# Optimization experiments

Hardware: AMD Instinct MI355X
Metric: run time of the kernel (lower is better)

The kernel has to match this reference:

```python
import jax, jax.numpy as jnp
import numpy as np

DIM = 1024
HEADS = 16
HEAD_DIM = DIM // HEADS
SCALE = HEAD_DIM ** -0.5
EPS = 1e-5


def layernorm(x, g, b):
    mu = jnp.mean(x, axis=-1, keepdims=True)
    var = jnp.mean((x - mu) ** 2, axis=-1, keepdims=True)
    return (x - mu) * jax.lax.rsqrt(var + EPS) * g + b


def setup_inputs() -> dict:
    key = jax.random.key(0)
    ks = jax.random.split(key, 12)
    B, N = 2, 2048
    s = DIM ** -0.5
    return {
        "q": jax.random.normal(ks[0], (B, N, DIM), jnp.float32),
        "k": jax.random.normal(ks[1], (B, N, DIM), jnp.float32),
        "v": jax.random.normal(ks[2], (B, N, DIM), jnp.float32),
        "gq": jnp.ones((DIM,), jnp.float32), "bq_ln": jnp.zeros((DIM,), jnp.float32),
        "gk": jnp.ones((DIM,), jnp.float32), "bk_ln": jnp.zeros((DIM,), jnp.float32),
        "gv": jnp.ones((DIM,), jnp.float32), "bv_ln": jnp.zeros((DIM,), jnp.float32),
        "Wq": jax.random.normal(ks[3], (DIM, DIM), jnp.float32) * s,
        "bq": jnp.zeros((DIM,), jnp.float32),
        "Wk": jax.random.normal(ks[4], (DIM, DIM), jnp.float32) * s,
        "bk": jnp.zeros((DIM,), jnp.float32),
        "Wv": jax.random.normal(ks[5], (DIM, DIM), jnp.float32) * s,
        "bv": jnp.zeros((DIM,), jnp.float32),
        "Wp": jax.random.normal(ks[6], (DIM, DIM), jnp.float32) * s,
        "bp": jnp.zeros((DIM,), jnp.float32),
    }


def reference(q, k, v, gq, bq_ln, gk, bk_ln, gv, bv_ln, Wq, bq, Wk, bk, Wv, bv, Wp, bp):
    B, Nq, C = q.shape
    Nk, Nv = k.shape[1], v.shape[1]
    qn = layernorm(q, gq, bq_ln)
    kn = layernorm(k, gk, bk_ln)
    vn = layernorm(v, gv, bv_ln)
    # project and split heads -> [B, H, N, hd]
    qh = (qn @ Wq + bq).reshape(B, Nq, HEADS, HEAD_DIM).transpose(0, 2, 1, 3)
    kh = (kn @ Wk + bk).reshape(B, Nk, HEADS, HEAD_DIM).transpose(0, 2, 1, 3)
    vh = (vn @ Wv + bv).reshape(B, Nv, HEADS, HEAD_DIM).transpose(0, 2, 1, 3)
    attn = jnp.einsum("bhqd,bhkd->bhqk", qh, kh) * SCALE
    attn = jax.nn.softmax(attn, axis=-1)
    out = jnp.einsum("bhqk,bhkd->bhqd", attn, vh)
    out = out.transpose(0, 2, 1, 3).reshape(B, Nq, C)
    out = out @ Wp + bp
    return (out, kh, vh)
```

## Files before the change

kernel.cpp:

```cpp
#include <hip/hip_runtime.h>
#include <cstdint>

#define DIMC 1024
#define NSEQ 2048
#define BATCH 2
#define HEADS 16
#define HD 64
#define MROWS (BATCH * NSEQ)

typedef unsigned short u16;
typedef unsigned int u32;
typedef __attribute__((ext_vector_type(8))) short bf16x8;
typedef __attribute__((ext_vector_type(4))) float f32x4;

#if __has_builtin(__builtin_amdgcn_exp2f)
#define EXP2(x) __builtin_amdgcn_exp2f(x)
#else
#define EXP2(x) exp2f(x)
#endif

__device__ __forceinline__ u16 f2bf(float f) {
  union { float f; u32 u; } v; v.f = f;
  u32 u = v.u;
  return (u16)((u + 0x7fffu + ((u >> 16) & 1u)) >> 16);
}
__device__ __forceinline__ u32 pack_rne(float a, float b) {
  return (u32)f2bf(a) | ((u32)f2bf(b) << 16);
}
__device__ __forceinline__ u32 pack_trunc(float a, float b) {
  union { float f; u32 u; } x, y; x.f = a; y.f = b;
  return (x.u >> 16) | (y.u & 0xffff0000u);
}
__device__ __forceinline__ void gload_lds16(const void* g, void* l) {
  __builtin_amdgcn_global_load_lds((const __attribute__((address_space(1))) void*)g,
                                   (__attribute__((address_space(3))) void*)l, 16, 0, 0);
}

__global__ __launch_bounds__(256)
void prep(const float* __restrict__ q, const float* __restrict__ k,
          const float* __restrict__ v,
          const float* __restrict__ gq, const float* __restrict__ bq,
          const float* __restrict__ gk, const float* __restrict__ bk,
          const float* __restrict__ gv, const float* __restrict__ bv,
          const float* __restrict__ w0, const float* __restrict__ w1,
          const float* __restrict__ w2, const float* __restrict__ w3,
          u16* __restrict__ xn, u16* __restrict__ wtout) {
  __shared__ float rs[4], rs2[4];
  __shared__ float tile[32][33];
  int tid = threadIdx.x;
  if (blockIdx.x < 3 * MROWS) {
    int rowid = blockIdx.x;
    int tensor = rowid >> 12;
    int r = rowid & 4095;
    const float *src, *g, *b;
    if (tensor == 0)      { src = q; g = gq; b = bq; }
    else if (tensor == 1) { src = k; g = gk; b = bk; }
    else                  { src = v; g = gv; b = bv; }
    src += (size_t)r * DIMC;
    u16* dst = xn + (size_t)tensor * MROWS * DIMC + (size_t)r * DIMC;
    float4 x = ((const float4*)src)[tid];
    float s  = x.x + x.y + x.z + x.w;
    float s2 = x.x*x.x + x.y*x.y + x.z*x.z + x.w*x.w;
    #pragma unroll
    for (int m = 1; m < 64; m <<= 1) { s += __shfl_xor(s, m); s2 += __shfl_xor(s2, m); }
    int wave = tid >> 6, lane = tid & 63;
    if (lane == 0) { rs[wave] = s; rs2[wave] = s2; }
    __syncthreads();
    s  = rs[0] + rs[1] + rs[2] + rs[3];
    s2 = rs2[0] + rs2[1] + rs2[2] + rs2[3];
    float mu  = s * (1.0f / DIMC);
    float var = s2 * (1.0f / DIMC) - mu * mu;
    float inv = rsqrtf(var + 1e-5f);
    float4 gg = ((const float4*)g)[tid];
    float4 bb = ((const float4*)b)[tid];
    uint2 o;
    o.x = pack_rne((x.x - mu) * inv * gg.x + bb.x, (x.y - mu) * inv * gg.y + bb.y);
    o.y = pack_rne((x.z - mu) * inv * gg.z + bb.z, (x.w - mu) * inv * gg.w + bb.w);
    ((uint2*)dst)[tid] = o;
  } else {
    int blk = blockIdx.x - 3 * MROWS;
    int widx = blk >> 10, t = blk & 1023;
    int ti = t >> 5, tj = t & 31;
    const float* W = (widx == 0) ? w0 : (widx == 1) ? w1 : (widx == 2) ? w2 : w3;
    u16* O = wtout + (size_t)widx * DIMC * DIMC;
    int tx = tid & 31, ty = tid >> 5;
    #pragma unroll
    for (int rr = 0; rr < 32; rr += 8)
      tile[ty + rr][tx] = W[(size_t)(ti * 32 + ty + rr) * DIMC + tj * 32 + tx];
    __syncthreads();
    #pragma unroll
    for (int rr = 0; rr < 32; rr += 8)
      O[(size_t)(tj * 32 + ty + rr) * DIMC + ti * 32 + tx] = f2bf(tile[tx][ty + rr]);
  }
}

__global__ __launch_bounds__(256)
void qkv_gemm(const u16* __restrict__ xn, const u16* __restrict__ wt,
              const float* __restrict__ bq, const float* __restrict__ bk,
              const float* __restrict__ bv,
              float* __restrict__ out, u16* __restrict__ qh,
              u16* __restrict__ khb, u16* __restrict__ vtb) {
  __shared__ u16 smem[128 * 136];
  u16* As = smem;
  u16* Bs = smem + 4096;
  u16* Ls = smem;
  const int z = blockIdx.z;
  const u16* A  = xn + (size_t)z * MROWS * DIMC;
  const u16* Bt = wt + (size_t)z * DIMC * DIMC;
  const float* bias = (z == 0) ? bq : (z == 1) ? bk : bv;
  const int bm = blockIdx.x, bn = blockIdx.y;
  const int tid = threadIdx.x;
  const int wave = tid >> 6, lane = tid & 63;
  const int wm = (wave & 1) * 64, wn = (wave >> 1) * 64;
  const int row = lane & 15, quad = lane >> 4;
  const float QSCL = 0.18033688011112042f;
  f32x4 acc[4][4] = {};
  for (int k0 = 0; k0 < DIMC; k0 += 32) {
    #pragma unroll
    for (int c = 0; c < 2; ++c) {
      int e = c * 2048 + tid * 8;
      int rr = e >> 5, col = e & 31;
      gload_lds16(&A[(size_t)(bm * 128 + rr) * DIMC + k0 + col], &As[e]);
      gload_lds16(&Bt[(size_t)(bn * 128 + rr) * DIMC + k0 + col], &Bs[e]);
    }
    __syncthreads();
    bf16x8 a[4], b[4];
    #pragma unroll
    for (int i = 0; i < 4; ++i)
      a[i] = *(const bf16x8*)(&As[(wm + i * 16 + row) * 32 + quad * 8]);
    #pragma unroll
    for (int j = 0; j < 4; ++j)
      b[j] = *(const bf16x8*)(&Bs[(wn + j * 16 + row) * 32 + quad * 8]);
    #pragma unroll
    for (int i = 0; i < 4; ++i)
      #pragma unroll
      for (int j = 0; j < 4; ++j)
        acc[i][j] = __builtin_amdgcn_mfma_f32_16x16x32_bf16(a[i], b[j], acc[i][j], 0, 0, 0);
    __syncthreads();
  }
  #pragma unroll
  for (int i = 0; i < 4; ++i) {
    #pragma unroll
    for (int j = 0; j < 4; ++j) {
      float val[4];
      #pragma unroll
      for (int r = 0; r < 4; ++r) {
        int m = bm * 128 + wm + i * 16 + quad * 4 + r;
        int c = bn * 128 + wn + j * 16 + row;
        val[r] = acc[i][j][r] + bias[c];
        int b_ = m >> 11, n = m & 2047, h = c >> 6, d = c & 63;
        int bh = b_ * HEADS + h;
        size_t hidx = ((size_t)bh * NSEQ + n) * HD + d;
        if (z == 0) {
          qh[hidx] = f2bf(val[r] * QSCL);
        } else {
          out[(size_t)z * MROWS * DIMC + hidx] = val[r];
          if (z == 1) khb[hidx] = f2bf(val[r]);
        }
      }
      if (z == 2) {
        int ct = wn + j * 16 + row;
        int mt = wm + i * 16 + quad * 4;
        u32* L = (u32*)(&Ls[ct * 136 + mt]);
        L[0] = pack_rne(val[0], val[1]);
        L[1] = pack_rne(val[2], val[3]);
      }
    }
  }
  if (z == 2) {
    __syncthreads();
    int b_ = (bm * 128) >> 11;
    int nbase = (bm * 128) & 2047;
    #pragma unroll
    for (int it = 0; it < 8; ++it) {
      int idx = it * 256 + tid;
      int ct = idx >> 4, ch = idx & 15;
      uint4 y = *(const uint4*)(&Ls[ct * 136 + ch * 8]);
      int c = bn * 128 + ct;
      int h = c >> 6, d = c & 63;
      size_t o = ((size_t)(b_ * HEADS + h) * HD + d) * NSEQ + nbase + ch * 8;
      *(uint4*)(&vtb[o]) = y;
    }
  }
}

__global__ __launch_bounds__(256)
void out_gemm(const u16* __restrict__ A, const u16* __restrict__ Bt,
              const float* __restrict__ bias, float* __restrict__ outf) {
  __shared__ u16 As[64 * 32];
  __shared__ u16 Bs[128 * 32];
  const int bm = blockIdx.x, bn = blockIdx.y;
  const int tid = threadIdx.x;
  const int wave = tid >> 6, lane = tid & 63;
  const int wm = (wave & 1) * 32, wn = (wave >> 1) * 64;
  const int row = lane & 15, quad = lane >> 4;
  f32x4 acc[2][4] = {};
  for (int k0 = 0; k0 < DIMC; k0 += 32) {
    {
      int e = tid * 8;
      int rr = e >> 5, col = e & 31;
      gload_lds16(&A[(size_t)(bm * 64 + rr) * DIMC + k0 + col], &As[e]);
    }
    #pragma unroll
    for (int c = 0; c < 2; ++c) {
      int e = c * 2048 + tid * 8;
      int rr = e >> 5, col = e & 31;
      gload_lds16(&Bt[(size_t)(bn * 128 + rr) * DIMC + k0 + col], &Bs[e]);
    }
    __syncthreads();
    bf16x8 a[2], b[4];
    #pragma unroll
    for (int i = 0; i < 2; ++i)
      a[i] = *(const bf16x8*)(&As[(wm + i * 16 + row) * 32 + quad * 8]);
    #pragma unroll
    for (int j = 0; j < 4; ++j)
      b[j] = *(const bf16x8*)(&Bs[(wn + j * 16 + row) * 32 + quad * 8]);
    #pragma unroll
    for (int i = 0; i < 2; ++i)
      #pragma unroll
      for (int j = 0; j < 4; ++j)
        acc[i][j] = __builtin_amdgcn_mfma_f32_16x16x32_bf16(a[i], b[j], acc[i][j], 0, 0, 0);
    __syncthreads();
  }
  #pragma unroll
  for (int i = 0; i < 2; ++i)
    #pragma unroll
    for (int j = 0; j < 4; ++j)
      #pragma unroll
      for (int r = 0; r < 4; ++r) {
        int m = bm * 64 + wm + i * 16 + quad * 4 + r;
        int c = bn * 128 + wn + j * 16 + row;
        outf[(size_t)m * DIMC + c] = acc[i][j][r] + bias[c];
      }
}

__global__ __launch_bounds__(256)
void attn_fused(const u16* __restrict__ qh, const u16* __restrict__ kh,
                const u16* __restrict__ vt, u16* __restrict__ ao) {
  __shared__ u16 Ks[128 * 64];
  __shared__ u16 Vs[64 * 128];
  __shared__ u16 Ps[4][16 * 40];
  const int qtile = blockIdx.x;
  const int bh = blockIdx.y;
  const int b = bh >> 4, h = bh & 15;
  const int tid = threadIdx.x;
  const int wave = tid >> 6, lane = tid & 63;
  const int qi = lane & 15, quad = lane >> 4;
  const int sw = qi & 7;
  const size_t base = (size_t)bh * NSEQ * HD;
  bf16x8 qf[2];
  {
    int qrow = qtile * 64 + wave * 16 + qi;
    #pragma unroll
    for (int kc = 0; kc < 2; ++kc)
      qf[kc] = *(const bf16x8*)(&qh[base + (size_t)qrow * HD + kc * 32 + quad * 8]);
  }
  float li = 0.f;
  f32x4 oacc[4] = {};
  u16* myPs = &Ps[wave][0];
  for (int kt = 0; kt < NSEQ / 128; ++kt) {
    __syncthreads();
    #pragma unroll
    for (int c = 0; c < 4; ++c) {
      int p = c * 256 + tid;
      int rk = p >> 3, ck = p & 7;
      gload_lds16(&kh[base + (size_t)(kt * 128 + rk) * HD + (ck ^ (rk & 7)) * 8], &Ks[p * 8]);
      int rv = p >> 4, cv = p & 15;
      gload_lds16(&vt[base + (size_t)rv * NSEQ + kt * 128 + (cv ^ (rv & 15)) * 8], &Vs[p * 8]);
    }
    __syncthreads();
    #pragma unroll
    for (int kc = 0; kc < 4; ++kc) {
      f32x4 s0 = {}, s1 = {};
      {
        const u16* kr0 = &Ks[((kc * 2) * 16 + qi) * 64];
        s0 = __builtin_amdgcn_mfma_f32_16x16x32_bf16(
            *(const bf16x8*)(&kr0[(quad ^ sw) * 8]), qf[0], s0, 0, 0, 0);
        s0 = __builtin_amdgcn_mfma_f32_16x16x32_bf16(
            *(const bf16x8*)(&kr0[((4 + quad) ^ sw) * 8]), qf[1], s0, 0, 0, 0);
        const u16* kr1 = &Ks[((kc * 2 + 1) * 16 + qi) * 64];
        s1 = __builtin_amdgcn_mfma_f32_16x16x32_bf16(
            *(const bf16x8*)(&kr1[(quad ^ sw) * 8]), qf[0], s1, 0, 0, 0);
        s1 = __builtin_amdgcn_mfma_f32_16x16x32_bf16(
            *(const bf16x8*)(&kr1[((4 + quad) ^ sw) * 8]), qf[1], s1, 0, 0, 0);
      }
      float p0 = EXP2(s0[0]), p1 = EXP2(s0[1]), p2 = EXP2(s0[2]), p3 = EXP2(s0[3]);
      float p4 = EXP2(s1[0]), p5 = EXP2(s1[1]), p6 = EXP2(s1[2]), p7 = EXP2(s1[3]);
      float psum = ((p0 + p1) + (p2 + p3)) + ((p4 + p5) + (p6 + p7));
      {
        u32* w0 = (u32*)(&myPs[qi * 40 + quad * 4]);
        w0[0] = pack_trunc(p0, p1);
        w0[1] = pack_trunc(p2, p3);
        u32* w1 = (u32*)(&myPs[qi * 40 + 16 + quad * 4]);
        w1[0] = pack_trunc(p4, p5);
        w1[1] = pack_trunc(p6, p7);
      }
      psum += __shfl_xor(psum, 16);
      psum += __shfl_xor(psum, 32);
      li += psum;
      asm volatile("" ::: "memory");
      bf16x8 pf = *(const bf16x8*)(&myPs[qi * 40 + quad * 8]);
      #pragma unroll
      for (int dt = 0; dt < 4; ++dt) {
        bf16x8 vf = *(const bf16x8*)(&Vs[(dt * 16 + qi) * 128 + ((kc * 4 + quad) ^ qi) * 8]);
        oacc[dt] = __builtin_amdgcn_mfma_f32_16x16x32_bf16(vf, pf, oacc[dt], 0, 0, 0);
      }
    }
  }
  {
    float inv = 1.0f / li;
    int token = b * NSEQ + qtile * 64 + wave * 16 + qi;
    #pragma unroll
    for (int dt = 0; dt < 4; ++dt) {
      int col = h * 64 + dt * 16 + quad * 4;
      *(u32*)(&ao[(size_t)token * DIMC + col])     = pack_rne(oacc[dt][0] * inv, oacc[dt][1] * inv);
      *(u32*)(&ao[(size_t)token * DIMC + col + 2]) = pack_rne(oacc[dt][2] * inv, oacc[dt][3] * inv);
    }
  }
}

extern "C" void kernel_launch(void* const* d_in, const int* in_sizes, int n_in,
                              void* d_out, int out_size, void* d_ws, size_t ws_size,
                              hipStream_t stream) {
  const float* q    = (const float*)d_in[0];
  const float* k    = (const float*)d_in[1];
  const float* v    = (const float*)d_in[2];
  const float* gq   = (const float*)d_in[3];
  const float* bqln = (const float*)d_in[4];
  const float* gk   = (const float*)d_in[5];
  const float* bkln = (const float*)d_in[6];
  const float* gv   = (const float*)d_in[7];
  const float* bvln = (const float*)d_in[8];
  const float* Wq   = (const float*)d_in[9];
  const float* bq   = (const float*)d_in[10];
  const float* Wk   = (const float*)d_in[11];
  const float* bk   = (const float*)d_in[12];
  const float* Wv   = (const float*)d_in[13];
  const float* bv   = (const float*)d_in[14];
  const float* Wp   = (const float*)d_in[15];
  const float* bp   = (const float*)d_in[16];
  float* out = (float*)d_out;

  char* ws = (char*)d_ws;
  u16* xn  = (u16*)(ws);
  u16* wt  = (u16*)(ws + (size_t)25165824);
  u16* qh  = (u16*)(ws + (size_t)33554432);
  u16* khb = (u16*)(ws + (size_t)41943040);
  u16* ao  = (u16*)(ws + (size_t)50331648);
  u16* vtb = (u16*)d_out;

  const size_t WEL = (size_t)DIMC * DIMC;

  prep<<<3 * MROWS + 4096, 256, 0, stream>>>(q, k, v, gq, bqln, gk, bkln, gv, bvln,
                                             Wq, Wk, Wv, Wp, xn, wt);
  qkv_gemm<<<dim3(MROWS / 128, DIMC / 128, 3), 256, 0, stream>>>(
      xn, wt, bq, bk, bv, out, qh, khb, vtb);
  attn_fused<<<dim3(NSEQ / 64, BATCH * HEADS), 256, 0, stream>>>(qh, khb, vtb, ao);
  out_gemm<<<dim3(MROWS / 64, DIMC / 128), 256, 0, stream>>>(ao, wt + 3 * WEL, bp, out);
}
```

Measured before the change: 253.0 us.

## Keep softmax probabilities in registers, permute V fragment loads, add MFMA priority hints

New measurement: 268.2 us. 1.06x slower.

```diff
diff --git a/kernel.cpp b/kernel.cpp
--- a/kernel.cpp
+++ b/kernel.cpp
@@ -11,6 +11,7 @@
 typedef unsigned short u16;
 typedef unsigned int u32;
 typedef __attribute__((ext_vector_type(8))) short bf16x8;
+typedef __attribute__((ext_vector_type(4))) short bf16x4;
 typedef __attribute__((ext_vector_type(4))) float f32x4;
 
 #if __has_builtin(__builtin_amdgcn_exp2f)
@@ -239,7 +240,6 @@
                 const u16* __restrict__ vt, u16* __restrict__ ao) {
   __shared__ u16 Ks[128 * 64];
   __shared__ u16 Vs[64 * 128];
-  __shared__ u16 Ps[4][16 * 40];
   const int qtile = blockIdx.x;
   const int bh = blockIdx.y;
   const int b = bh >> 4, h = bh & 15;
@@ -257,7 +257,6 @@
   }
   float li = 0.f;
   f32x4 oacc[4] = {};
-  u16* myPs = &Ps[wave][0];
   for (int kt = 0; kt < NSEQ / 128; ++kt) {
     __syncthreads();
     #pragma unroll
@@ -271,40 +270,45 @@
     __syncthreads();
     #pragma unroll
     for (int kc = 0; kc < 4; ++kc) {
+      const u16* kr0 = &Ks[((kc * 2) * 16 + qi) * 64];
+      const u16* kr1 = &Ks[((kc * 2 + 1) * 16 + qi) * 64];
+      bf16x8 k0a = *(const bf16x8*)(&kr0[(quad ^ sw) * 8]);
+      bf16x8 k0b = *(const bf16x8*)(&kr0[((4 + quad) ^ sw) * 8]);
+      bf16x8 k1a = *(const bf16x8*)(&kr1[(quad ^ sw) * 8]);
+      bf16x8 k1b = *(const bf16x8*)(&kr1[((4 + quad) ^ sw) * 8]);
+      bf16x8 vfr[4];
+      #pragma unroll
+      for (int dt = 0; dt < 4; ++dt) {
+        const u16* vrow = &Vs[(dt * 16 + qi) * 128];
+        int c0 = (kc * 4 + (quad >> 1)) ^ qi;
+        int c1 = (kc * 4 + 2 + (quad >> 1)) ^ qi;
+        bf16x4 vlo = *(const bf16x4*)(&vrow[c0 * 8 + (quad & 1) * 4]);
+        bf16x4 vhi = *(const bf16x4*)(&vrow[c1 * 8 + (quad & 1) * 4]);
+        vfr[dt] = __builtin_shufflevector(vlo, vhi, 0, 1, 2, 3, 4, 5, 6, 7);
+      }
       f32x4 s0 = {}, s1 = {};
-      {
-        const u16* kr0 = &Ks[((kc * 2) * 16 + qi) * 64];
-        s0 = __builtin_amdgcn_mfma_f32_16x16x32_bf16(
-            *(const bf16x8*)(&kr0[(quad ^ sw) * 8]), qf[0], s0, 0, 0, 0);
-        s0 = __builtin_amdgcn_mfma_f32_16x16x32_bf16(
-            *(const bf16x8*)(&kr0[((4 + quad) ^ sw) * 8]), qf[1], s0, 0, 0, 0);
-        const u16* kr1 = &Ks[((kc * 2 + 1) * 16 + qi) * 64];
-        s1 = __builtin_amdgcn_mfma_f32_16x16x32_bf16(
-            *(const bf16x8*)(&kr1[(quad ^ sw) * 8]), qf[0], s1, 0, 0, 0);
-        s1 = __builtin_amdgcn_mfma_f32_16x16x32_bf16(
-            *(const bf16x8*)(&kr1[((4 + quad) ^ sw) * 8]), qf[1], s1, 0, 0, 0);
-      }
+      __builtin_amdgcn_s_setprio(1);
+      s0 = __builtin_amdgcn_mfma_f32_16x16x32_bf16(k0a, qf[0], s0, 0, 0, 0);
+      s0 = __builtin_amdgcn_mfma_f32_16x16x32_bf16(k0b, qf[1], s0, 0, 0, 0);
+      s1 = __builtin_amdgcn_mfma_f32_16x16x32_bf16(k1a, qf[0], s1, 0, 0, 0);
+      s1 = __builtin_amdgcn_mfma_f32_16x16x32_bf16(k1b, qf[1], s1, 0, 0, 0);
+      __builtin_amdgcn_s_setprio(0);
       float p0 = EXP2(s0[0]), p1 = EXP2(s0[1]), p2 = EXP2(s0[2]), p3 = EXP2(s0[3]);
       float p4 = EXP2(s1[0]), p5 = EXP2(s1[1]), p6 = EXP2(s1[2]), p7 = EXP2(s1[3]);
       float psum = ((p0 + p1) + (p2 + p3)) + ((p4 + p5) + (p6 + p7));
-      {
-        u32* w0 = (u32*)(&myPs[qi * 40 + quad * 4]);
-        w0[0] = pack_trunc(p0, p1);
-        w0[1] = pack_trunc(p2, p3);
-        u32* w1 = (u32*)(&myPs[qi * 40 + 16 + quad * 4]);
-        w1[0] = pack_trunc(p4, p5);
-        w1[1] = pack_trunc(p6, p7);
-      }
       psum += __shfl_xor(psum, 16);
       psum += __shfl_xor(psum, 32);
       li += psum;
-      asm volatile("" ::: "memory");
-      bf16x8 pf = *(const bf16x8*)(&myPs[qi * 40 + quad * 8]);
-      #pragma unroll
-      for (int dt = 0; dt < 4; ++dt) {
-        bf16x8 vf = *(const bf16x8*)(&Vs[(dt * 16 + qi) * 128 + ((kc * 4 + quad) ^ qi) * 8]);
-        oacc[dt] = __builtin_amdgcn_mfma_f32_16x16x32_bf16(vf, pf, oacc[dt], 0, 0, 0);
-      }
+      union { bf16x8 v; u32 u[4]; } pu;
+      pu.u[0] = pack_trunc(p0, p1);
+      pu.u[1] = pack_trunc(p2, p3);
+      pu.u[2] = pack_trunc(p4, p5);
+      pu.u[3] = pack_trunc(p6, p7);
+      __builtin_amdgcn_s_setprio(1);
+      #pragma unroll
+      for (int dt = 0; dt < 4; ++dt)
+        oacc[dt] = __builtin_amdgcn_mfma_f32_16x16x32_bf16(vfr[dt], pu.v, oacc[dt], 0, 0, 0);
+      __builtin_amdgcn_s_setprio(0);
     }
   }
   {
```

## Double-buffer K/V tiles in attention, remap blocks across heads, add MFMA priority

Applied to the files above, without the earlier changes.

After: 256.3 us. No clear change (+1.3%).

```diff
diff --git a/kernel.cpp b/kernel.cpp
--- a/kernel.cpp
+++ b/kernel.cpp
@@ -237,11 +237,12 @@
 __global__ __launch_bounds__(256)
 void attn_fused(const u16* __restrict__ qh, const u16* __restrict__ kh,
                 const u16* __restrict__ vt, u16* __restrict__ ao) {
-  __shared__ u16 Ks[128 * 64];
-  __shared__ u16 Vs[64 * 128];
+  __shared__ u16 Ks[2][64 * 64];
+  __shared__ u16 Vs[2][64 * 64];
   __shared__ u16 Ps[4][16 * 40];
-  const int qtile = blockIdx.x;
-  const int bh = blockIdx.y;
+  const int flat = blockIdx.x;
+  const int bh = (flat & 7) * 4 + ((flat >> 3) & 3);
+  const int qtile = flat >> 5;
   const int b = bh >> 4, h = bh & 15;
   const int tid = threadIdx.x;
   const int wave = tid >> 6, lane = tid & 63;
@@ -255,34 +256,48 @@
     for (int kc = 0; kc < 2; ++kc)
       qf[kc] = *(const bf16x8*)(&qh[base + (size_t)qrow * HD + kc * 32 + quad * 8]);
   }
+  #pragma unroll
+  for (int c = 0; c < 2; ++c) {
+    int p = c * 256 + tid;
+    int rk = p >> 3, ck = p & 7;
+    gload_lds16(&kh[base + (size_t)rk * HD + (ck ^ (rk & 7)) * 8], &Ks[0][p * 8]);
+    gload_lds16(&vt[base + (size_t)rk * NSEQ + (ck ^ (rk & 7)) * 8], &Vs[0][p * 8]);
+  }
+  __syncthreads();
   float li = 0.f;
   f32x4 oacc[4] = {};
   u16* myPs = &Ps[wave][0];
-  for (int kt = 0; kt < NSEQ / 128; ++kt) {
-    __syncthreads();
-    #pragma unroll
-    for (int c = 0; c < 4; ++c) {
-      int p = c * 256 + tid;
-      int rk = p >> 3, ck = p & 7;
-      gload_lds16(&kh[base + (size_t)(kt * 128 + rk) * HD + (ck ^ (rk & 7)) * 8], &Ks[p * 8]);
-      int rv = p >> 4, cv = p & 15;
-      gload_lds16(&vt[base + (size_t)rv * NSEQ + kt * 128 + (cv ^ (rv & 15)) * 8], &Vs[p * 8]);
-    }
-    __syncthreads();
-    #pragma unroll
-    for (int kc = 0; kc < 4; ++kc) {
+  for (int t = 0; t < NSEQ / 64; ++t) {
+    const int cur = t & 1;
+    if (t < NSEQ / 64 - 1) {
+      #pragma unroll
+      for (int c = 0; c < 2; ++c) {
+        int p = c * 256 + tid;
+        int rk = p >> 3, ck = p & 7;
+        gload_lds16(&kh[base + (size_t)((t + 1) * 64 + rk) * HD + (ck ^ (rk & 7)) * 8],
+                    &Ks[cur ^ 1][p * 8]);
+        gload_lds16(&vt[base + (size_t)rk * NSEQ + (t + 1) * 64 + (ck ^ (rk & 7)) * 8],
+                    &Vs[cur ^ 1][p * 8]);
+      }
+    }
+    const u16* Kb = &Ks[cur][0];
+    const u16* Vb = &Vs[cur][0];
+    #pragma unroll
+    for (int kc = 0; kc < 2; ++kc) {
       f32x4 s0 = {}, s1 = {};
       {
-        const u16* kr0 = &Ks[((kc * 2) * 16 + qi) * 64];
+        const u16* kr0 = &Kb[((kc * 2) * 16 + qi) * 64];
+        const u16* kr1 = &Kb[((kc * 2 + 1) * 16 + qi) * 64];
+        __builtin_amdgcn_s_setprio(1);
         s0 = __builtin_amdgcn_mfma_f32_16x16x32_bf16(
             *(const bf16x8*)(&kr0[(quad ^ sw) * 8]), qf[0], s0, 0, 0, 0);
         s0 = __builtin_amdgcn_mfma_f32_16x16x32_bf16(
             *(const bf16x8*)(&kr0[((4 + quad) ^ sw) * 8]), qf[1], s0, 0, 0, 0);
-        const u16* kr1 = &Ks[((kc * 2 + 1) * 16 + qi) * 64];
         s1 = __builtin_amdgcn_mfma_f32_16x16x32_bf16(
             *(const bf16x8*)(&kr1[(quad ^ sw) * 8]), qf[0], s1, 0, 0, 0);
         s1 = __builtin_amdgcn_mfma_f32_16x16x32_bf16(
             *(const bf16x8*)(&kr1[((4 + quad) ^ sw) * 8]), qf[1], s1, 0, 0, 0);
+        __builtin_amdgcn_s_setprio(0);
       }
       float p0 = EXP2(s0[0]), p1 = EXP2(s0[1]), p2 = EXP2(s0[2]), p3 = EXP2(s0[3]);
       float p4 = EXP2(s1[0]), p5 = EXP2(s1[1]), p6 = EXP2(s1[2]), p7 = EXP2(s1[3]);
@@ -300,12 +315,15 @@
       li += psum;
       asm volatile("" ::: "memory");
       bf16x8 pf = *(const bf16x8*)(&myPs[qi * 40 + quad * 8]);
+      __builtin_amdgcn_s_setprio(1);
       #pragma unroll
       for (int dt = 0; dt < 4; ++dt) {
-        bf16x8 vf = *(const bf16x8*)(&Vs[(dt * 16 + qi) * 128 + ((kc * 4 + quad) ^ qi) * 8]);
+        bf16x8 vf = *(const bf16x8*)(&Vb[(dt * 16 + qi) * 64 + ((kc * 4 + quad) ^ sw) * 8]);
         oacc[dt] = __builtin_amdgcn_mfma_f32_16x16x32_bf16(vf, pf, oacc[dt], 0, 0, 0);
       }
-    }
+      __builtin_amdgcn_s_setprio(0);
+    }
+    __syncthreads();
   }
   {
     float inv = 1.0f / li;
@@ -355,6 +373,6 @@
                                              Wq, Wk, Wv, Wp, xn, wt);
   qkv_gemm<<<dim3(MROWS / 128, DIMC / 128, 3), 256, 0, stream>>>(
       xn, wt, bq, bk, bv, out, qh, khb, vtb);
-  attn_fused<<<dim3(NSEQ / 64, BATCH * HEADS), 256, 0, stream>>>(qh, khb, vtb, ao);
+  attn_fused<<<dim3((NSEQ / 64) * BATCH * HEADS), 256, 0, stream>>>(qh, khb, vtb, ao);
   out_gemm<<<dim3(MROWS / 64, DIMC / 128), 256, 0, stream>>>(ao, wt + 3 * WEL, bp, out);
 }
```
